# Performance work log

Hardware: AMD Instinct MI355X
Metric: run time of the kernel (lower is better)

Reference implementation:

```python
import jax, jax.numpy as jnp
import numpy as np

EMB = 1024
NH = 16
HS = EMB // NH  # 64


def setup_inputs() -> dict:
    key = jax.random.key(0)
    k_x, k_wqkv, k_bqkv, k_wo, k_bo = jax.random.split(key, 5)
    x = jax.random.normal(k_x, (4, 2048, EMB), dtype=jnp.float32)
    s = 1.0 / np.sqrt(EMB)
    # torch nn.Linear weight is [out, in]; store as [in, out] for x @ W
    w_qkv = jax.random.uniform(k_wqkv, (EMB, 3 * EMB), dtype=jnp.float32, minval=-s, maxval=s)
    b_qkv = jax.random.uniform(k_bqkv, (3 * EMB,), dtype=jnp.float32, minval=-s, maxval=s)
    w_out = jax.random.uniform(k_wo, (EMB, EMB), dtype=jnp.float32, minval=-s, maxval=s)
    b_out = jax.random.uniform(k_bo, (EMB,), dtype=jnp.float32, minval=-s, maxval=s)
    return {"x": x, "w_qkv": w_qkv, "b_qkv": b_qkv, "w_out": w_out, "b_out": b_out}


def reference(x, w_qkv, b_qkv, w_out, b_out):
    B, T, C = x.shape
    qkv = x @ w_qkv + b_qkv  # [B, T, 3*C]
    q, k, v = jnp.split(qkv, 3, axis=-1)
    # [B, T, C] -> [B, nh, T, hs]
    def heads(t):
        return t.reshape(B, T, NH, HS).transpose(0, 2, 1, 3)
    q, k, v = heads(q), heads(k), heads(v)
    scores = jnp.einsum('bhqd,bhkd->bhqk', q, k) / jnp.sqrt(jnp.float32(HS))
    attn = jax.nn.softmax(scores, axis=-1)  # dropout=0 -> identity
    out = jnp.einsum('bhqk,bhkd->bhqd', attn, v)
    out = out.transpose(0, 2, 1, 3).reshape(B, T, NH * HS)
    return out @ w_out + b_out
```

## Files before the change

### kernel.cpp

```cpp
#include <hip/hip_runtime.h>

typedef unsigned short u16;
typedef unsigned int u32;
typedef __attribute__((ext_vector_type(8))) __bf16 bf16x8;
typedef __attribute__((ext_vector_type(4))) __bf16 bf16x4;
typedef __attribute__((ext_vector_type(4))) float f32x4;

#define GLD_AS1 const __attribute__((address_space(1))) void*
#define GLD_AS3 __attribute__((address_space(3))) void*

__device__ __forceinline__ u16 f2b(float f) {
  u32 u = __builtin_bit_cast(u32, f);
  u += 0x7fffu + ((u >> 16) & 1u);
  return (u16)(u >> 16);
}

__global__ void transpose_w_kernel(const float* __restrict__ src, u16* __restrict__ dst,
                                   int R, int C) {
  __shared__ float tile[32][33];
  int c0 = blockIdx.x * 32, r0 = blockIdx.y * 32;
  int tx = threadIdx.x & 31, ty = threadIdx.x >> 5;
  #pragma unroll
  for (int i = ty; i < 32; i += 8)
    tile[i][tx] = src[(size_t)(r0 + i) * C + c0 + tx];
  __syncthreads();
  #pragma unroll
  for (int i = ty; i < 32; i += 8)
    dst[(size_t)(c0 + i) * R + r0 + tx] = f2b(tile[tx][i]);
}

__global__ void transpose_v_kernel(const u16* __restrict__ v, u16* __restrict__ vt) {
  __shared__ u16 tile[64][68];
  int t0 = blockIdx.x * 64;
  int bh = blockIdx.y;
  int tx = threadIdx.x & 31, ty = threadIdx.x >> 5;
  const u16* src = v + (size_t)bh * 2048 * 64;
  u16* dst = vt + (size_t)bh * 64 * 2048;
  #pragma unroll
  for (int i = ty; i < 64; i += 8)
    *(u32*)&tile[i][tx * 2] = *(const u32*)&src[(size_t)(t0 + i) * 64 + tx * 2];
  __syncthreads();
  const int c = tx * 2;
  const int e = c & 3, g = (c >> 2) & 3, hi = (c >> 4) & 1;
  const int cp = (c & 32) | (8 * g + 4 * hi + e);
  #pragma unroll
  for (int d = ty; d < 64; d += 8) {
    u32 a = tile[c][d];
    u32 b = tile[c + 1][d];
    *(u32*)&dst[(size_t)d * 2048 + t0 + cp] = a | (b << 16);
  }
}

template <int MODE>
__global__ __launch_bounds__(256)
void gemm_kernel(const void* __restrict__ Ap, const u16* __restrict__ Bt,
                 const float* __restrict__ bias,
                 u16* __restrict__ qo, u16* __restrict__ ko, u16* __restrict__ vo,
                 float* __restrict__ outF, int N, int K) {
  __shared__ char As[(MODE == 0) ? 32768 : 16384];
  __shared__ char Bs[16384];
  const int tid = threadIdx.x;
  const int lane = tid & 63, wave = tid >> 6;
  const int m0 = blockIdx.x * 128, n0 = blockIdx.y * 128;
  const int wm = (wave >> 1) * 64, wn = (wave & 1) * 64;
  const int lr = lane & 15, lg = lane >> 4;

  const int rB = tid >> 3;
  const int cB = ((tid & 7) * 16) ^ ((rB & 7) << 4);
  const int rA16 = tid >> 4;
  const int cA = ((tid & 15) * 16) ^ (rA16 << 4);

  const size_t strideA = (size_t)K * (MODE == 0 ? 4 : 2);
  const size_t strideB = (size_t)K * 2;
  const char* Ab = (const char*)Ap + (size_t)m0 * strideA;
  const char* Bb = (const char*)(Bt + (size_t)n0 * K);

  f32x4 acc[4][4] = {};
  const int swr = (lr & 7) << 4;

  const int nk = K >> 6;
  for (int kt = 0; kt < nk; ++kt) {
    if (MODE == 0) {
      #pragma unroll
      for (int i = 0; i < 8; ++i)
        __builtin_amdgcn_global_load_lds(
            (GLD_AS1)(Ab + (size_t)(i * 16 + rA16) * strideA + kt * 256 + cA),
            (GLD_AS3)(As + i * 4096 + tid * 16), 16, 0, 0);
    } else {
      #pragma unroll
      for (int i = 0; i < 4; ++i)
        __builtin_amdgcn_global_load_lds(
            (GLD_AS1)(Ab + (size_t)(i * 32 + rB) * strideA + kt * 128 + cB),
            (GLD_AS3)(As + i * 4096 + tid * 16), 16, 0, 0);
    }
    #pragma unroll
    for (int i = 0; i < 4; ++i)
      __builtin_amdgcn_global_load_lds(
          (GLD_AS1)(Bb + (size_t)(i * 32 + rB) * strideB + kt * 128 + cB),
          (GLD_AS3)(Bs + i * 4096 + tid * 16), 16, 0, 0);
    __syncthreads();

    bf16x8 af[4][2], bfr[4][2];
    #pragma unroll
    for (int m = 0; m < 4; ++m) {
      const int row = wm + m * 16 + lr;
      #pragma unroll
      for (int s = 0; s < 2; ++s) {
        if (MODE == 0) {
          f32x4 a0 = *(const f32x4*)(As + row * 256 + ((s * 128 + lg * 32) ^ (lr << 4)));
          f32x4 a1 = *(const f32x4*)(As + row * 256 + ((s * 128 + lg * 32 + 16) ^ (lr << 4)));
          bf16x8 v;
          #pragma unroll
          for (int e = 0; e < 4; ++e) { v[e] = (__bf16)a0[e]; v[4 + e] = (__bf16)a1[e]; }
          af[m][s] = v;
        } else {
          af[m][s] = *(const bf16x8*)(As + row * 128 + ((s * 64 + lg * 16) ^ swr));
        }
      }
    }
    #pragma unroll
    for (int n = 0; n < 4; ++n) {
      const int row = wn + n * 16 + lr;
      #pragma unroll
      for (int s = 0; s < 2; ++s)
        bfr[n][s] = *(const bf16x8*)(Bs + row * 128 + ((s * 64 + lg * 16) ^ swr));
    }
    __builtin_amdgcn_s_setprio(1);
    #pragma unroll
    for (int m = 0; m < 4; ++m)
      #pragma unroll
      for (int n = 0; n < 4; ++n) {
        acc[m][n] = __builtin_amdgcn_mfma_f32_16x16x32_bf16(af[m][0], bfr[n][0], acc[m][n], 0, 0, 0);
        acc[m][n] = __builtin_amdgcn_mfma_f32_16x16x32_bf16(af[m][1], bfr[n][1], acc[m][n], 0, 0, 0);
      }
    __builtin_amdgcn_s_setprio(0);
    __syncthreads();
  }

  #pragma unroll
  for (int n = 0; n < 4; ++n) {
    const int col = n0 + wn + n * 16 + lr;
    const float bv = bias[col];
    #pragma unroll
    for (int m = 0; m < 4; ++m) {
      const int rowb = m0 + wm + m * 16 + lg * 4;
      #pragma unroll
      for (int j = 0; j < 4; ++j) {
        float val = acc[m][n][j] + bv;
        int row = rowb + j;
        if (MODE == 0) {
          int which = col >> 10, c = col & 1023;
          int h = c >> 6, d = c & 63;
          int b = row >> 11, t = row & 2047;
          if (which == 0) val *= 0.18033688011112042f;
          u16* dst = which == 0 ? qo : (which == 1 ? ko : vo);
          dst[((size_t)(b * 16 + h) * 2048 + t) * 64 + d] = f2b(val);
        } else {
          outF[(size_t)row * N + col] = val;
        }
      }
    }
  }
}

__global__ __launch_bounds__(512)
void attn_kernel(const u16* __restrict__ Q, const u16* __restrict__ Kg,
                 const u16* __restrict__ Vt, u16* __restrict__ att) {
  const int tid = threadIdx.x;
  const int wave = tid >> 6, lane = tid & 63;
  const int lr = lane & 15, lg = lane >> 4;
  const int bh = blockIdx.x;
  const int q0 = blockIdx.y * 256;
  const int b = bh >> 4, h = bh & 15;

  const u16* Qh = Q + (size_t)bh * 2048 * 64;
  const char* Khb = (const char*)(Kg + (size_t)bh * 2048 * 64);
  const char* Vhb = (const char*)(Vt + (size_t)bh * 64 * 2048);

  __shared__ u16 Ks[3][64 * 64];
  __shared__ u16 Vs[3][64 * 64];

  const int rS = tid >> 3;
  const int cS = ((tid & 7) * 16) ^ ((rS & 7) << 4);

  bf16x8 qf[2][2];
  #pragma unroll
  for (int m = 0; m < 2; ++m)
    #pragma unroll
    for (int s = 0; s < 2; ++s)
      qf[m][s] = *(const bf16x8*)(Qh + (size_t)(q0 + wave * 32 + m * 16 + lr) * 64 + s * 32 + lg * 8);

  bf16x8 ones;
  #pragma unroll
  for (int e = 0; e < 8; ++e) ones[e] = (__bf16)1.0f;

  f32x4 acc[2][4] = {};
  f32x4 accl[2] = {};

#define STAGE(T, BUF)                                                          \
  {                                                                            \
    __builtin_amdgcn_global_load_lds(                                          \
        (GLD_AS1)(Khb + (size_t)((T) * 64 + rS) * 128 + cS),                   \
        (GLD_AS3)((char*)Ks[BUF] + tid * 16), 16, 0, 0);                       \
    __builtin_amdgcn_global_load_lds(                                          \
        (GLD_AS1)(Vhb + (size_t)rS * 4096 + (T) * 128 + cS),                   \
        (GLD_AS3)((char*)Vs[BUF] + tid * 16), 16, 0, 0);                       \
  }

  STAGE(0, 0);
  STAGE(1, 1);

  for (int kt = 0; kt < 32; ++kt) {
    if (kt == 31) { asm volatile("s_waitcnt vmcnt(0)" ::: "memory"); }
    else          { asm volatile("s_waitcnt vmcnt(2)" ::: "memory"); }
    __builtin_amdgcn_sched_barrier(0);
    __builtin_amdgcn_s_barrier();
    if (kt < 30) STAGE(kt + 2, (kt + 2) % 3);
    const int cur = kt % 3;

    #pragma unroll
    for (int ks = 0; ks < 2; ++ks) {
      f32x4 sf0[2] = {}, sf1[2] = {};
      __builtin_amdgcn_s_setprio(1);
      #pragma unroll
      for (int s = 0; s < 2; ++s) {
        bf16x8 kf0 = *(const bf16x8*)((const char*)Ks[cur] + (2 * ks * 16 + lr) * 128 +
                                      ((s * 64 + lg * 16) ^ ((lr & 7) << 4)));
        sf0[0] = __builtin_amdgcn_mfma_f32_16x16x32_bf16(kf0, qf[0][s], sf0[0], 0, 0, 0);
        sf0[1] = __builtin_amdgcn_mfma_f32_16x16x32_bf16(kf0, qf[1][s], sf0[1], 0, 0, 0);
        bf16x8 kf1 = *(const bf16x8*)((const char*)Ks[cur] + ((2 * ks + 1) * 16 + lr) * 128 +
                                      ((s * 64 + lg * 16) ^ ((lr & 7) << 4)));
        sf1[0] = __builtin_amdgcn_mfma_f32_16x16x32_bf16(kf1, qf[0][s], sf1[0], 0, 0, 0);
        sf1[1] = __builtin_amdgcn_mfma_f32_16x16x32_bf16(kf1, qf[1][s], sf1[1], 0, 0, 0);
      }
      __builtin_amdgcn_s_setprio(0);

      bf16x8 pa[2];
      #pragma unroll
      for (int m = 0; m < 2; ++m)
        #pragma unroll
        for (int j = 0; j < 4; ++j) {
          pa[m][j]     = (__bf16)__builtin_amdgcn_exp2f(sf0[m][j]);
          pa[m][4 + j] = (__bf16)__builtin_amdgcn_exp2f(sf1[m][j]);
        }

      __builtin_amdgcn_s_setprio(1);
      accl[0] = __builtin_amdgcn_mfma_f32_16x16x32_bf16(ones, pa[0], accl[0], 0, 0, 0);
      accl[1] = __builtin_amdgcn_mfma_f32_16x16x32_bf16(ones, pa[1], accl[1], 0, 0, 0);
      #pragma unroll
      for (int d = 0; d < 4; ++d) {
        const int rv = d * 16 + lr;
        bf16x8 vf = *(const bf16x8*)((const char*)Vs[cur] + rv * 128 +
                                     ((64 * ks + 16 * lg) ^ ((lr & 7) << 4)));
        acc[0][d] = __builtin_amdgcn_mfma_f32_16x16x32_bf16(vf, pa[0], acc[0][d], 0, 0, 0);
        acc[1][d] = __builtin_amdgcn_mfma_f32_16x16x32_bf16(vf, pa[1], acc[1][d], 0, 0, 0);
      }
      __builtin_amdgcn_s_setprio(0);
    }
  }

  #pragma unroll
  for (int m = 0; m < 2; ++m) {
    const float inv = 1.0f / accl[m][0];
    const int t = q0 + wave * 32 + m * 16 + lr;
    #pragma unroll
    for (int d = 0; d < 4; ++d) {
      bf16x4 ov;
      #pragma unroll
      for (int j = 0; j < 4; ++j) ov[j] = (__bf16)(acc[m][d][j] * inv);
      *(bf16x4*)&att[((size_t)b * 2048 + t) * 1024 + h * 64 + d * 16 + lg * 4] = ov;
    }
  }
#undef STAGE
}

extern "C" void kernel_launch(void* const* d_in, const int* in_sizes, int n_in,
                              void* d_out, int out_size, void* d_ws, size_t ws_size,
                              hipStream_t stream) {
  const float* x     = (const float*)d_in[0];
  const float* w_qkv = (const float*)d_in[1];
  const float* b_qkv = (const float*)d_in[2];
  const float* w_out = (const float*)d_in[3];
  const float* b_out = (const float*)d_in[4];
  float* out = (float*)d_out;

  char* ws = (char*)d_ws;
  const size_t MB = 1024 * 1024;
  u16* attb  = (u16*)(ws);
  u16* wqkvt = (u16*)(ws + 16 * MB);
  u16* woutt = (u16*)(ws + 22 * MB);
  u16* qb    = (u16*)(ws + 24 * MB);
  u16* kb    = (u16*)(ws + 40 * MB);
  u16* vb    = (u16*)(ws + 56 * MB);
  u16* vtb   = (u16*)(ws + 72 * MB);

  transpose_w_kernel<<<dim3(3072 / 32, 1024 / 32), 256, 0, stream>>>(w_qkv, wqkvt, 1024, 3072);
  transpose_w_kernel<<<dim3(1024 / 32, 1024 / 32), 256, 0, stream>>>(w_out, woutt, 1024, 1024);

  gemm_kernel<0><<<dim3(8192 / 128, 3072 / 128), 256, 0, stream>>>(
      x, wqkvt, b_qkv, qb, kb, vb, nullptr, 3072, 1024);

  transpose_v_kernel<<<dim3(2048 / 64, 64), 256, 0, stream>>>(vb, vtb);

  attn_kernel<<<dim3(64, 8), 512, 0, stream>>>(qb, kb, vtb, attb);

  gemm_kernel<1><<<dim3(8192 / 128, 1024 / 128), 256, 0, stream>>>(
      attb, woutt, b_out, nullptr, nullptr, nullptr, out, 1024, 1024);
}
```

Baseline: 183.8 us.

## Fuse V transpose into QKV GEMM epilogue and remap workgroups for XCD locality

The QKV GEMM epilogue now writes V straight into the transposed, permuted layout the attention kernel expects, using 4-element vector stores. This removes the separate transpose_v kernel launch and its extra read/write pass over V. Both GEMMs also remap block IDs so that consecutive workgroups are grouped across the 8 XCDs, which should improve L2 reuse. The trade-off is that V stores are now strided by 2048 elements per column, so the epilogue writes are less coalesced.

```diff
diff --git a/kernel.cpp b/kernel.cpp
--- a/kernel.cpp
+++ b/kernel.cpp
@@ -27,28 +27,6 @@
   #pragma unroll
   for (int i = ty; i < 32; i += 8)
     dst[(size_t)(c0 + i) * R + r0 + tx] = f2b(tile[tx][i]);
-}
-
-__global__ void transpose_v_kernel(const u16* __restrict__ v, u16* __restrict__ vt) {
-  __shared__ u16 tile[64][68];
-  int t0 = blockIdx.x * 64;
-  int bh = blockIdx.y;
-  int tx = threadIdx.x & 31, ty = threadIdx.x >> 5;
-  const u16* src = v + (size_t)bh * 2048 * 64;
-  u16* dst = vt + (size_t)bh * 64 * 2048;
-  #pragma unroll
-  for (int i = ty; i < 64; i += 8)
-    *(u32*)&tile[i][tx * 2] = *(const u32*)&src[(size_t)(t0 + i) * 64 + tx * 2];
-  __syncthreads();
-  const int c = tx * 2;
-  const int e = c & 3, g = (c >> 2) & 3, hi = (c >> 4) & 1;
-  const int cp = (c & 32) | (8 * g + 4 * hi + e);
-  #pragma unroll
-  for (int d = ty; d < 64; d += 8) {
-    u32 a = tile[c][d];
-    u32 b = tile[c + 1][d];
-    *(u32*)&dst[(size_t)d * 2048 + t0 + cp] = a | (b << 16);
-  }
 }
 
 template <int MODE>
@@ -61,7 +39,13 @@
   __shared__ char Bs[16384];
   const int tid = threadIdx.x;
   const int lane = tid & 63, wave = tid >> 6;
-  const int m0 = blockIdx.x * 128, n0 = blockIdx.y * 128;
+
+  const int nwg = gridDim.x * gridDim.y;
+  const int orig = blockIdx.x + gridDim.x * blockIdx.y;
+  const int wgid = (orig & 7) * (nwg >> 3) + (orig >> 3);
+  const int bx = wgid % gridDim.x, by = wgid / gridDim.x;
+
+  const int m0 = bx * 128, n0 = by * 128;
   const int wm = (wave >> 1) * 64, wn = (wave & 1) * 64;
   const int lr = lane & 15, lg = lane >> 4;
 
@@ -137,27 +121,48 @@
     __syncthreads();
   }
 
-  #pragma unroll
-  for (int n = 0; n < 4; ++n) {
-    const int col = n0 + wn + n * 16 + lr;
-    const float bv = bias[col];
-    #pragma unroll
-    for (int m = 0; m < 4; ++m) {
-      const int rowb = m0 + wm + m * 16 + lg * 4;
-      #pragma unroll
-      for (int j = 0; j < 4; ++j) {
-        float val = acc[m][n][j] + bv;
-        int row = rowb + j;
-        if (MODE == 0) {
-          int which = col >> 10, c = col & 1023;
-          int h = c >> 6, d = c & 63;
-          int b = row >> 11, t = row & 2047;
-          if (which == 0) val *= 0.18033688011112042f;
-          u16* dst = which == 0 ? qo : (which == 1 ? ko : vo);
-          dst[((size_t)(b * 16 + h) * 2048 + t) * 64 + d] = f2b(val);
+  if (MODE == 0) {
+    const int b = m0 >> 11;
+    #pragma unroll
+    for (int n = 0; n < 4; ++n) {
+      const int col = n0 + wn + n * 16 + lr;
+      const float bv = bias[col];
+      const int which = col >> 10, c = col & 1023;
+      const int h = c >> 6, d = c & 63;
+      #pragma unroll
+      for (int m = 0; m < 4; ++m) {
+        const int rowb = m0 + wm + m * 16 + lg * 4;
+        const int t0 = rowb & 2047;
+        if (which == 2) {
+          const int tp = (t0 & ~31) | (8 * ((t0 >> 2) & 3) + 4 * ((t0 >> 4) & 1));
+          ushort4 q4;
+          q4.x = f2b(acc[m][n][0] + bv);
+          q4.y = f2b(acc[m][n][1] + bv);
+          q4.z = f2b(acc[m][n][2] + bv);
+          q4.w = f2b(acc[m][n][3] + bv);
+          *(ushort4*)&vo[((size_t)(b * 16 + h) * 64 + d) * 2048 + tp] = q4;
         } else {
-          outF[(size_t)row * N + col] = val;
+          u16* dst = (which == 0) ? qo : ko;
+          const float scl = (which == 0) ? 0.18033688011112042f : 1.0f;
+          #pragma unroll
+          for (int j = 0; j < 4; ++j) {
+            float val = (acc[m][n][j] + bv) * scl;
+            dst[((size_t)(b * 16 + h) * 2048 + (t0 + j)) * 64 + d] = f2b(val);
+          }
         }
+      }
+    }
+  } else {
+    #pragma unroll
+    for (int n = 0; n < 4; ++n) {
+      const int col = n0 + wn + n * 16 + lr;
+      const float bv = bias[col];
+      #pragma unroll
+      for (int m = 0; m < 4; ++m) {
+        const int rowb = m0 + wm + m * 16 + lg * 4;
+        #pragma unroll
+        for (int j = 0; j < 4; ++j)
+          outF[(size_t)(rowb + j) * N + col] = acc[m][n][j] + bv;
       }
     }
   }
@@ -291,16 +296,13 @@
   u16* woutt = (u16*)(ws + 22 * MB);
   u16* qb    = (u16*)(ws + 24 * MB);
   u16* kb    = (u16*)(ws + 40 * MB);
-  u16* vb    = (u16*)(ws + 56 * MB);
-  u16* vtb   = (u16*)(ws + 72 * MB);
+  u16* vtb   = (u16*)(ws + 56 * MB);
 
   transpose_w_kernel<<<dim3(3072 / 32, 1024 / 32), 256, 0, stream>>>(w_qkv, wqkvt, 1024, 3072);
   transpose_w_kernel<<<dim3(1024 / 32, 1024 / 32), 256, 0, stream>>>(w_out, woutt, 1024, 1024);
 
   gemm_kernel<0><<<dim3(8192 / 128, 3072 / 128), 256, 0, stream>>>(
-      x, wqkvt, b_qkv, qb, kb, vb, nullptr, 3072, 1024);
-
-  transpose_v_kernel<<<dim3(2048 / 64, 64), 256, 0, stream>>>(vb, vtb);
+      x, wqkvt, b_qkv, qb, kb, vtb, nullptr, 3072, 1024);
 
   attn_kernel<<<dim3(64, 8), 512, 0, stream>>>(qb, kb, vtb, attb);
 
```

Measured after the change: 224.3 us. +22.0%, slower.
